# Kernel tuning notes

Hardware: AMD Instinct MI355X
Metric: run time of the kernel (lower is better)

Reference implementation:

```python
import jax, jax.numpy as jnp
import numpy as np

BN_EPS = 1e-5


def setup_inputs() -> dict:
    key = jax.random.key(0)
    ks = jax.random.split(key, 6)
    N, F, H, C, E = 50000, 128, 256, 40, 800000
    x = jax.random.normal(ks[0], (N, F), dtype=jnp.float32)
    edge_index = jax.random.randint(ks[1], (2, E), 0, N, dtype=jnp.int64)
    eps = jnp.zeros((), dtype=jnp.float32)  # train_eps=True, init 0
    W1 = jax.random.normal(ks[2], (F, H), dtype=jnp.float32) * (1.0 / np.sqrt(F))
    b1 = jnp.zeros((H,), dtype=jnp.float32)
    gamma = jnp.ones((H,), dtype=jnp.float32)
    beta = jnp.zeros((H,), dtype=jnp.float32)
    W2 = jax.random.normal(ks[3], (H, C), dtype=jnp.float32) * (1.0 / np.sqrt(H))
    b2 = jnp.zeros((C,), dtype=jnp.float32)
    return {"x": x, "edge_index": edge_index, "eps": eps, "W1": W1, "b1": b1,
            "gamma": gamma, "beta": beta, "W2": W2, "b2": b2}


def reference(x, edge_index, eps, W1, b1, gamma, beta, W2, b2):
    N = x.shape[0]
    src, dst = edge_index[0], edge_index[1]  # source_to_target flow
    # GIN sum aggregation: sum_{j in N(i)} x_j  (scatter-add over edges)
    agg = jax.ops.segment_sum(x[src], dst, num_segments=N)
    h = (1.0 + eps) * x + agg  # [N, F]
    # MLP: Linear -> ReLU (act_first) -> BatchNorm -> Linear (plain last)
    h = jax.nn.relu(h @ W1 + b1)  # [N, H]
    mean = jnp.mean(h, axis=0)
    var = jnp.var(h, axis=0)  # biased var, training-mode batch norm
    h = (h - mean) * jax.lax.rsqrt(var + BN_EPS) * gamma + beta
    out = h @ W2 + b2  # [N, C]
    return jax.nn.log_softmax(out, axis=-1)
```

## Files before the change

kernel.cpp:

```cpp
#include <hip/hip_runtime.h>
#include <hip/hip_bf16.h>
#include <math.h>

#define F_IN 128
#define H_DIM 256
#define C_OUT 40

typedef __attribute__((ext_vector_type(8))) short short8v;
typedef __attribute__((ext_vector_type(4))) float float4v;

__device__ __forceinline__ unsigned short f2bf(float f) {
    union { float f; unsigned int u; } c; c.f = f;
    unsigned int r = (c.u + 0x7fffu + ((c.u >> 16) & 1u)) >> 16;
    return (unsigned short)r;
}
__device__ __forceinline__ float bf2f(unsigned short u) {
    union { unsigned int u; float f; } c; c.u = ((unsigned int)u) << 16;
    return c.f;
}

__global__ __launch_bounds__(256) void prep(const float* __restrict__ x,
                                            const float* __restrict__ W1,
                                            unsigned short* __restrict__ x_b,
                                            unsigned short* __restrict__ w1t,
                                            int* __restrict__ head,
                                            float* __restrict__ sums,
                                            float* __restrict__ sumsq,
                                            int N, int nA) {
    int b = blockIdx.x;
    if (b < nA) {
        long long i = ((long long)b * 256 + threadIdx.x) * 8;
        if (i + 7 < (long long)N * F_IN) {
            float4 v0 = *reinterpret_cast<const float4*>(x + i);
            float4 v1 = *reinterpret_cast<const float4*>(x + i + 4);
            short8v o;
            o[0] = (short)f2bf(v0.x); o[1] = (short)f2bf(v0.y);
            o[2] = (short)f2bf(v0.z); o[3] = (short)f2bf(v0.w);
            o[4] = (short)f2bf(v1.x); o[5] = (short)f2bf(v1.y);
            o[6] = (short)f2bf(v1.z); o[7] = (short)f2bf(v1.w);
            *reinterpret_cast<short8v*>(x_b + i) = o;
        }
    } else if (b == nA) {
        int t = threadIdx.x;
        for (int k = 0; k < F_IN; ++k)
            w1t[t * F_IN + k] = f2bf(W1[(size_t)k * H_DIM + t]);
        sums[t] = 0.f;
        sumsq[t] = 0.f;
    } else {
        int i = (b - nA - 1) * 256 + threadIdx.x;
        if (i < N) head[i] = -1;
    }
}

__global__ __launch_bounds__(256) void build_list(const int* __restrict__ src,
                                                  const int* __restrict__ dst,
                                                  int* __restrict__ head,
                                                  int2* __restrict__ listbuf, int E) {
    int i = blockIdx.x * 256 + threadIdx.x;
    if (i >= E) return;
    int d = dst[i];
    int prev = atomicExch(&head[d], i);
    listbuf[i] = make_int2(src[i], prev);
}

__global__ __launch_bounds__(256) void gather_agg(const unsigned short* __restrict__ xb,
                                                  const float* __restrict__ epsp,
                                                  const int* __restrict__ head,
                                                  const int2* __restrict__ listbuf,
                                                  unsigned short* __restrict__ aggb, int N) {
    int wave = (blockIdx.x * 256 + (int)threadIdx.x) >> 6;
    int lane = threadIdx.x & 63;
    int g = lane >> 4;
    int lr = lane & 15;
    int node = wave * 4 + g;
    bool valid = node < N;
    int j = valid ? head[node] : -1;

    float acc[8] = {};
    while (__any(j >= 0)) {
        if (j >= 0) {
            int2 e = listbuf[j];
            short8v v = *reinterpret_cast<const short8v*>(xb + (size_t)e.x * F_IN + lr * 8);
            j = e.y;
            #pragma unroll
            for (int t = 0; t < 8; ++t) acc[t] += bf2f((unsigned short)v[t]);
        }
    }

    if (valid) {
        float sc = 1.0f + epsp[0];
        short8v xv = *reinterpret_cast<const short8v*>(xb + (size_t)node * F_IN + lr * 8);
        short8v o;
        #pragma unroll
        for (int t = 0; t < 8; ++t)
            o[t] = (short)f2bf(fmaf(sc, bf2f((unsigned short)xv[t]), acc[t]));
        *reinterpret_cast<short8v*>(aggb + (size_t)node * F_IN + lr * 8) = o;
    }
}

__global__ __launch_bounds__(256) void gemm1_mfma(const unsigned short* __restrict__ agg_b,
                                                  const unsigned short* __restrict__ w1t,
                                                  const float* __restrict__ b1,
                                                  unsigned short* __restrict__ h1,
                                                  float* __restrict__ sums,
                                                  float* __restrict__ sumsq, int N) {
    __shared__ short As[128][136];
    __shared__ short Bs[64][136];
    __shared__ float sums_l[64], ssq_l[64];

    int tid = threadIdx.x;
    int m0 = blockIdx.x * 128;
    int n0 = blockIdx.y * 64;

    if (tid < 64) { sums_l[tid] = 0.f; ssq_l[tid] = 0.f; }

    #pragma unroll
    for (int i = 0; i < 8; ++i) {
        int c = tid + i * 256;
        int row = c >> 4, ck = c & 15;
        int gr = m0 + row;
        short8v v = {0, 0, 0, 0, 0, 0, 0, 0};
        if (gr < N) v = *reinterpret_cast<const short8v*>(agg_b + (size_t)gr * F_IN + ck * 8);
        *reinterpret_cast<short8v*>(&As[row][ck * 8]) = v;
    }
    #pragma unroll
    for (int i = 0; i < 4; ++i) {
        int c = tid + i * 256;
        int row = c >> 4, ck = c & 15;
        *reinterpret_cast<short8v*>(&Bs[row][ck * 8]) =
            *reinterpret_cast<const short8v*>(w1t + (size_t)(n0 + row) * F_IN + ck * 8);
    }
    __syncthreads();

    int w = tid >> 6, lane = tid & 63;
    int wm = w >> 1, wn = w & 1;
    int lr = lane & 15, lk = (lane >> 4) * 8;

    float4v acc[4][2] = {};
    #pragma unroll
    for (int ks = 0; ks < 4; ++ks) {
        int k0 = ks * 32 + lk;
        short8v a[4], b[2];
        #pragma unroll
        for (int am = 0; am < 4; ++am)
            a[am] = *reinterpret_cast<short8v*>(&As[wm * 64 + am * 16 + lr][k0]);
        #pragma unroll
        for (int bn = 0; bn < 2; ++bn)
            b[bn] = *reinterpret_cast<short8v*>(&Bs[wn * 32 + bn * 16 + lr][k0]);
        #pragma unroll
        for (int am = 0; am < 4; ++am)
            #pragma unroll
            for (int bn = 0; bn < 2; ++bn)
                acc[am][bn] = __builtin_amdgcn_mfma_f32_16x16x32_bf16(a[am], b[bn], acc[am][bn], 0, 0, 0);
    }

    __syncthreads();
    short (*T)[72] = reinterpret_cast<short (*)[72]>(&As[0][0]);
    #pragma unroll
    for (int bn = 0; bn < 2; ++bn) {
        int col = wn * 32 + bn * 16 + lr;
        float bias = b1[n0 + col];
        float ps = 0.f, pss = 0.f;
        #pragma unroll
        for (int am = 0; am < 4; ++am) {
            #pragma unroll
            for (int r = 0; r < 4; ++r) {
                int rowl = wm * 64 + am * 16 + (lane >> 4) * 4 + r;
                float v = fmaxf(acc[am][bn][r] + bias, 0.f);
                unsigned short ub = f2bf(v);
                T[rowl][col] = (short)ub;
                if (m0 + rowl < N) {
                    float vr = bf2f(ub);
                    ps += vr;
                    pss = fmaf(vr, vr, pss);
                }
            }
        }
        atomicAdd(&sums_l[col], ps);
        atomicAdd(&ssq_l[col], pss);
    }
    __syncthreads();

    #pragma unroll
    for (int i = 0; i < 4; ++i) {
        int c = tid + i * 256;
        int row = c >> 3, ck = c & 7;
        int gr = m0 + row;
        if (gr < N)
            *reinterpret_cast<short8v*>(h1 + (size_t)gr * H_DIM + n0 + ck * 8) =
                *reinterpret_cast<short8v*>(&T[row][ck * 8]);
    }
    if (tid < 64) {
        atomicAdd(&sums[n0 + tid], sums_l[tid]);
        atomicAdd(&sumsq[n0 + tid], ssq_l[tid]);
    }
}

__global__ __launch_bounds__(256) void bn_fold(const float* __restrict__ sums,
                                               const float* __restrict__ sumsq,
                                               const float* __restrict__ gamma,
                                               const float* __restrict__ beta,
                                               const float* __restrict__ W2,
                                               const float* __restrict__ b2,
                                               unsigned short* __restrict__ w2frag,
                                               float* __restrict__ b2f, int N) {
    __shared__ float scale_s[H_DIM], shift_s[H_DIM];
    int k = threadIdx.x;
    float invN = 1.0f / (float)N;
    float mean = sums[k] * invN;
    float var = sumsq[k] * invN - mean * mean;
    float scale = gamma[k] * rsqrtf(var + 1e-5f);
    float shift = beta[k] - mean * scale;
    scale_s[k] = scale;
    shift_s[k] = shift;
    __syncthreads();
    if (k < 48) {
        if (k < C_OUT) {
            float acc = b2[k];
            for (int j = 0; j < H_DIM; ++j) acc = fmaf(shift_s[j], W2[j * C_OUT + k], acc);
            b2f[k] = acc;
        } else {
            b2f[k] = -1e30f;
        }
    }
    for (int u = threadIdx.x; u < 1536; u += 256) {
        int lane = u & 63, t = u >> 6;
        int ks = t / 3, bf = t - ks * 3;
        int col = bf * 16 + (lane & 15);
        int kb = ks * 32 + (lane >> 4) * 8;
        short8v o;
        #pragma unroll
        for (int e = 0; e < 8; ++e) {
            int kk = kb + e;
            float v = (col < C_OUT) ? scale_s[kk] * W2[kk * C_OUT + col] : 0.f;
            o[e] = (short)f2bf(v);
        }
        *reinterpret_cast<short8v*>(w2frag + (size_t)u * 8) = o;
    }
}

__global__ __launch_bounds__(256) void gemm2_lsm(const unsigned short* __restrict__ h1,
                                                 const unsigned short* __restrict__ w2frag,
                                                 const float* __restrict__ b2f,
                                                 float* __restrict__ out, int N) {
    int tid = threadIdx.x;
    int wm = tid >> 6;
    int lane = tid & 63;
    int lr = lane & 15;
    int g = lane >> 4;
    int row0 = blockIdx.x * 64 + wm * 16;
    int arow = row0 + lr;
    if (arow >= N) arow = N - 1;

    short8v a[8];
    const unsigned short* ap = h1 + (size_t)arow * H_DIM + g * 8;
    #pragma unroll
    for (int ks = 0; ks < 8; ++ks)
        a[ks] = *reinterpret_cast<const short8v*>(ap + ks * 32);

    float4v acc[3] = {};
    #pragma unroll
    for (int ks = 0; ks < 8; ++ks) {
        #pragma unroll
        for (int bf = 0; bf < 3; ++bf) {
            short8v b = *reinterpret_cast<const short8v*>(
                w2frag + (size_t)(((ks * 3 + bf) << 6) + lane) * 8);
            acc[bf] = __builtin_amdgcn_mfma_f32_16x16x32_bf16(a[ks], b, acc[bf], 0, 0, 0);
        }
    }

    float b0 = b2f[lr], b1v = b2f[16 + lr], b2v = b2f[32 + lr];
    #pragma unroll
    for (int r = 0; r < 4; ++r) {
        float v0 = acc[0][r] + b0;
        float v1 = acc[1][r] + b1v;
        float v2 = acc[2][r] + b2v;
        float m = fmaxf(fmaxf(v0, v1), v2);
        #pragma unroll
        for (int o = 1; o < 16; o <<= 1) m = fmaxf(m, __shfl_xor(m, o, 64));
        float s = __expf(v0 - m) + __expf(v1 - m) + __expf(v2 - m);
        #pragma unroll
        for (int o = 1; o < 16; o <<= 1) s += __shfl_xor(s, o, 64);
        float lse = m + __logf(s);
        int row = row0 + g * 4 + r;
        if (row < N) {
            float* op = out + (size_t)row * C_OUT;
            op[lr] = v0 - lse;
            op[16 + lr] = v1 - lse;
            if (lr < 8) op[32 + lr] = v2 - lse;
        }
    }
}

extern "C" void kernel_launch(void* const* d_in, const int* in_sizes, int n_in,
                              void* d_out, int out_size, void* d_ws, size_t ws_size,
                              hipStream_t stream) {
    const float* x     = (const float*)d_in[0];
    const int*   ei    = (const int*)d_in[1];
    const float* eps   = (const float*)d_in[2];
    const float* W1    = (const float*)d_in[3];
    const float* b1    = (const float*)d_in[4];
    const float* gamma = (const float*)d_in[5];
    const float* beta  = (const float*)d_in[6];
    const float* W2    = (const float*)d_in[7];
    const float* b2    = (const float*)d_in[8];
    float* out = (float*)d_out;

    int N = in_sizes[0] / F_IN;
    int E = in_sizes[1] / 2;
    const int* srcIdx = ei;
    const int* dstIdx = ei + E;

    unsigned short* x_b    = (unsigned short*)d_ws;
    unsigned short* agg_b  = x_b + (size_t)N * F_IN;
    unsigned short* w1t    = agg_b + (size_t)N * F_IN;
    unsigned short* h1     = w1t + H_DIM * F_IN;
    float* sums   = (float*)(h1 + (size_t)N * H_DIM);
    float* sumsq  = sums + H_DIM;
    unsigned short* w2frag = (unsigned short*)(sumsq + H_DIM);
    float* b2f    = (float*)(w2frag + 1536 * 8);

    int*  head    = (int*)h1;
    int2* listbuf = (int2*)(head + N);

    int nA = (N * 16 + 255) / 256;
    int nZ = (N + 255) / 256;
    hipLaunchKernelGGL(prep, dim3(nA + 1 + nZ), dim3(256), 0, stream,
                       x, W1, x_b, w1t, head, sums, sumsq, N, nA);

    hipLaunchKernelGGL(build_list, dim3((E + 255) / 256), dim3(256), 0, stream,
                       srcIdx, dstIdx, head, listbuf, E);

    hipLaunchKernelGGL(gather_agg, dim3((N + 15) / 16), dim3(256), 0, stream,
                       x_b, eps, head, listbuf, agg_b, N);

    dim3 g1((N + 127) / 128, H_DIM / 64);
    hipLaunchKernelGGL(gemm1_mfma, g1, dim3(256), 0, stream,
                       agg_b, w1t, b1, h1, sums, sumsq, N);

    hipLaunchKernelGGL(bn_fold, dim3(1), dim3(H_DIM), 0, stream,
                       sums, sumsq, gamma, beta, W2, b2, w2frag, b2f, N);

    hipLaunchKernelGGL(gemm2_lsm, dim3((N + 63) / 64), dim3(256), 0, stream,
                       h1, w2frag, b2f, out, N);
}
```

Before: 169.6 us.

## Parallelize W1 transpose, widen gather lanes, replace BN atomics with partials

The W1 transpose/convert, previously done by a single block looping over 128 k values, is spread across 128 blocks. The gather kernel now gives each node 8 lanes that each load 16 bf16 values, instead of 16 lanes loading 8, so each wave covers 8 nodes and has more independent loads in flight. BN statistics are written as per-block partials and reduced serially in bn_fold, which removes the global atomics and the zero-initialization. The trade-off is that the single-block bn_fold now loops over about 391 partial rows, and the wider per-node lane groups may make wave divergence worse on nodes with uneven degree.

```diff
diff --git a/kernel.cpp b/kernel.cpp
--- a/kernel.cpp
+++ b/kernel.cpp
@@ -24,8 +24,6 @@
                                             unsigned short* __restrict__ x_b,
                                             unsigned short* __restrict__ w1t,
                                             int* __restrict__ head,
-                                            float* __restrict__ sums,
-                                            float* __restrict__ sumsq,
                                             int N, int nA) {
     int b = blockIdx.x;
     if (b < nA) {
@@ -40,14 +38,12 @@
             o[6] = (short)f2bf(v1.z); o[7] = (short)f2bf(v1.w);
             *reinterpret_cast<short8v*>(x_b + i) = o;
         }
-    } else if (b == nA) {
-        int t = threadIdx.x;
-        for (int k = 0; k < F_IN; ++k)
-            w1t[t * F_IN + k] = f2bf(W1[(size_t)k * H_DIM + t]);
-        sums[t] = 0.f;
-        sumsq[t] = 0.f;
+    } else if (b < nA + 128) {
+        int t = (b - nA) * 2 + (threadIdx.x >> 7);
+        int k = threadIdx.x & 127;
+        w1t[t * F_IN + k] = f2bf(W1[(size_t)k * H_DIM + t]);
     } else {
-        int i = (b - nA - 1) * 256 + threadIdx.x;
+        int i = (b - nA - 128) * 256 + threadIdx.x;
         if (i < N) head[i] = -1;
     }
 }
@@ -70,31 +66,41 @@
                                                   unsigned short* __restrict__ aggb, int N) {
     int wave = (blockIdx.x * 256 + (int)threadIdx.x) >> 6;
     int lane = threadIdx.x & 63;
-    int g = lane >> 4;
-    int lr = lane & 15;
-    int node = wave * 4 + g;
+    int g = lane >> 3;
+    int lr = lane & 7;
+    int node = wave * 8 + g;
     bool valid = node < N;
     int j = valid ? head[node] : -1;
 
-    float acc[8] = {};
+    float acc[16] = {};
     while (__any(j >= 0)) {
         if (j >= 0) {
             int2 e = listbuf[j];
-            short8v v = *reinterpret_cast<const short8v*>(xb + (size_t)e.x * F_IN + lr * 8);
+            const unsigned short* rp = xb + (size_t)e.x * F_IN + lr * 16;
+            short8v v0 = *reinterpret_cast<const short8v*>(rp);
+            short8v v1 = *reinterpret_cast<const short8v*>(rp + 8);
             j = e.y;
             #pragma unroll
-            for (int t = 0; t < 8; ++t) acc[t] += bf2f((unsigned short)v[t]);
+            for (int t = 0; t < 8; ++t) acc[t] += bf2f((unsigned short)v0[t]);
+            #pragma unroll
+            for (int t = 0; t < 8; ++t) acc[8 + t] += bf2f((unsigned short)v1[t]);
         }
     }
 
     if (valid) {
         float sc = 1.0f + epsp[0];
-        short8v xv = *reinterpret_cast<const short8v*>(xb + (size_t)node * F_IN + lr * 8);
-        short8v o;
-        #pragma unroll
-        for (int t = 0; t < 8; ++t)
-            o[t] = (short)f2bf(fmaf(sc, bf2f((unsigned short)xv[t]), acc[t]));
-        *reinterpret_cast<short8v*>(aggb + (size_t)node * F_IN + lr * 8) = o;
+        const unsigned short* xp = xb + (size_t)node * F_IN + lr * 16;
+        short8v x0 = *reinterpret_cast<const short8v*>(xp);
+        short8v x1 = *reinterpret_cast<const short8v*>(xp + 8);
+        short8v o0, o1;
+        #pragma unroll
+        for (int t = 0; t < 8; ++t) {
+            o0[t] = (short)f2bf(fmaf(sc, bf2f((unsigned short)x0[t]), acc[t]));
+            o1[t] = (short)f2bf(fmaf(sc, bf2f((unsigned short)x1[t]), acc[8 + t]));
+        }
+        unsigned short* op = aggb + (size_t)node * F_IN + lr * 16;
+        *reinterpret_cast<short8v*>(op) = o0;
+        *reinterpret_cast<short8v*>(op + 8) = o1;
     }
 }
 
@@ -102,8 +108,7 @@
                                                   const unsigned short* __restrict__ w1t,
                                                   const float* __restrict__ b1,
                                                   unsigned short* __restrict__ h1,
-                                                  float* __restrict__ sums,
-                                                  float* __restrict__ sumsq, int N) {
+                                                  float* __restrict__ partials, int N) {
     __shared__ short As[128][136];
     __shared__ short Bs[64][136];
     __shared__ float sums_l[64], ssq_l[64];
@@ -191,13 +196,13 @@
                 *reinterpret_cast<short8v*>(&T[row][ck * 8]);
     }
     if (tid < 64) {
-        atomicAdd(&sums[n0 + tid], sums_l[tid]);
-        atomicAdd(&sumsq[n0 + tid], ssq_l[tid]);
-    }
-}
-
-__global__ __launch_bounds__(256) void bn_fold(const float* __restrict__ sums,
-                                               const float* __restrict__ sumsq,
+        size_t base = (size_t)blockIdx.x * 512;
+        partials[base + n0 + tid] = sums_l[tid];
+        partials[base + 256 + n0 + tid] = ssq_l[tid];
+    }
+}
+
+__global__ __launch_bounds__(256) void bn_fold(const float* __restrict__ partials, int nbx,
                                                const float* __restrict__ gamma,
                                                const float* __restrict__ beta,
                                                const float* __restrict__ W2,
@@ -206,9 +211,14 @@
                                                float* __restrict__ b2f, int N) {
     __shared__ float scale_s[H_DIM], shift_s[H_DIM];
     int k = threadIdx.x;
+    float s = 0.f, ss = 0.f;
+    for (int b = 0; b < nbx; ++b) {
+        s += partials[(size_t)b * 512 + k];
+        ss += partials[(size_t)b * 512 + 256 + k];
+    }
     float invN = 1.0f / (float)N;
-    float mean = sums[k] * invN;
-    float var = sumsq[k] * invN - mean * mean;
+    float mean = s * invN;
+    float var = ss * invN - mean * mean;
     float scale = gamma[k] * rsqrtf(var + 1e-5f);
     float shift = beta[k] - mean * scale;
     scale_s[k] = scale;
@@ -311,13 +321,14 @@
     const int* srcIdx = ei;
     const int* dstIdx = ei + E;
 
+    int nbx = (N + 127) / 128;
+
     unsigned short* x_b    = (unsigned short*)d_ws;
     unsigned short* agg_b  = x_b + (size_t)N * F_IN;
     unsigned short* w1t    = agg_b + (size_t)N * F_IN;
     unsigned short* h1     = w1t + H_DIM * F_IN;
-    float* sums   = (float*)(h1 + (size_t)N * H_DIM);
-    float* sumsq  = sums + H_DIM;
-    unsigned short* w2frag = (unsigned short*)(sumsq + H_DIM);
+    float* partials = (float*)(h1 + (size_t)N * H_DIM);
+    unsigned short* w2frag = (unsigned short*)(partials + (size_t)nbx * 512);
     float* b2f    = (float*)(w2frag + 1536 * 8);
 
     int*  head    = (int*)h1;
@@ -325,21 +336,21 @@
 
     int nA = (N * 16 + 255) / 256;
     int nZ = (N + 255) / 256;
-    hipLaunchKernelGGL(prep, dim3(nA + 1 + nZ), dim3(256), 0, stream,
-                       x, W1, x_b, w1t, head, sums, sumsq, N, nA);
+    hipLaunchKernelGGL(prep, dim3(nA + 128 + nZ), dim3(256), 0, stream,
+                       x, W1, x_b, w1t, head, N, nA);
 
     hipLaunchKernelGGL(build_list, dim3((E + 255) / 256), dim3(256), 0, stream,
                        srcIdx, dstIdx, head, listbuf, E);
 
-    hipLaunchKernelGGL(gather_agg, dim3((N + 15) / 16), dim3(256), 0, stream,
+    hipLaunchKernelGGL(gather_agg, dim3((N + 31) / 32), dim3(256), 0, stream,
                        x_b, eps, head, listbuf, agg_b, N);
 
-    dim3 g1((N + 127) / 128, H_DIM / 64);
+    dim3 g1(nbx, H_DIM / 64);
     hipLaunchKernelGGL(gemm1_mfma, g1, dim3(256), 0, stream,
-                       agg_b, w1t, b1, h1, sums, sumsq, N);
+                       agg_b, w1t, b1, h1, partials, N);
 
     hipLaunchKernelGGL(bn_fold, dim3(1), dim3(H_DIM), 0, stream,
-                       sums, sumsq, gamma, beta, W2, b2, w2frag, b2f, N);
+                       partials, nbx, gamma, beta, W2, b2, w2frag, b2f, N);
 
     hipLaunchKernelGGL(gemm2_lsm, dim3((N + 63) / 64), dim3(256), 0, stream,
                        h1, w2frag, b2f, out, N);
```

Result: slower. 235.2 us (+38.7%).
